# Kernel tuning notes

Hardware: AMD Instinct MI355X
Metric: run time of the kernel (lower is better)

The kernel has to match this reference:

```python
import jax, jax.numpy as jnp
import numpy as np

B, S, D = 8, 1024, 1024
H, KV, HD = 16, 16, 64
NDIM = 2
EPS = 1e-6


def rms_norm(x, weight=None, eps=EPS):
    var = jnp.mean(jnp.square(x), axis=-1, keepdims=True)
    out = x * jax.lax.rsqrt(var + eps)
    if weight is not None:
        out = out * weight
    return out


def rotate_half(x):
    half = x.shape[-1] // 2
    return jnp.concatenate((-x[..., half:], x[..., :half]), axis=-1)


def multidim_rope(x, cos, sin, ndim):
    # x: [B,S,H,HD]; cos,sin: [B,S,HD]; head_dim split into ndim contiguous
    # chunks of size per = 2*(HD // (2*ndim)); rotate-half applied per chunk.
    b, s, h, hd = x.shape
    per = 2 * (hd // (2 * ndim))
    xg = x.reshape(b, s, h, ndim, per)
    cg = cos.reshape(b, s, 1, ndim, per)
    sg = sin.reshape(b, s, 1, ndim, per)
    out = xg * cg + rotate_half(xg) * sg
    return out.reshape(b, s, h, hd)


def setup_inputs() -> dict:
    key = jax.random.key(0)
    ks = jax.random.split(key, 10)
    scale = 1.0 / np.sqrt(D)
    return {
        "hidden_states": jax.random.normal(ks[0], (B, S, D), jnp.float32),
        "cos": jax.random.uniform(ks[1], (B, S, HD), jnp.float32, -1.0, 1.0),
        "sin": jax.random.uniform(ks[2], (B, S, HD), jnp.float32, -1.0, 1.0),
        "position_ids": jax.random.randint(ks[3], (B, S, NDIM), 0, 32, jnp.int32),
        "wq": jax.random.normal(ks[4], (D, H * HD), jnp.float32) * scale,
        "wk": jax.random.normal(ks[5], (D, KV * HD), jnp.float32) * scale,
        "wv": jax.random.normal(ks[6], (D, KV * HD), jnp.float32) * scale,
        "wo": jax.random.normal(ks[7], (H * HD, D), jnp.float32) * scale,
        "q_norm_w": jnp.ones((HD,), jnp.float32),
        "k_norm_w": jnp.ones((HD,), jnp.float32),
    }


def reference(hidden_states, cos, sin, position_ids, wq, wk, wv, wo, q_norm_w, k_norm_w):
    b, s, _ = hidden_states.shape
    ndim = position_ids.shape[-1]

    q = (hidden_states @ wq).reshape(b, s, H, HD)
    q = rms_norm(q, q_norm_w)
    q = multidim_rope(q, cos, sin, ndim)

    k = (hidden_states @ wk).reshape(b, s, KV, HD)
    k = rms_norm(k, k_norm_w)
    k = multidim_rope(k, cos, sin, ndim)

    v = (hidden_states @ wv).reshape(b, s, KV, HD)
    v = rms_norm(v, None)  # v_norm has no weight

    # Full (non-causal) vision attention, scaling = 1.0
    scores = jnp.einsum("bqhd,bkhd->bhqk", q, k)
    probs = jax.nn.softmax(scores, axis=-1)
    attn = jnp.einsum("bhqk,bkhd->bqhd", probs, v).reshape(b, s, H * HD)

    return attn @ wo
```

## Files before the change

### kernel.cpp

```cpp
#include <hip/hip_runtime.h>
#include <hip/hip_bf16.h>

typedef __attribute__((ext_vector_type(8))) short bf16x8;
typedef __attribute__((ext_vector_type(4))) short bf16x4;
typedef __attribute__((ext_vector_type(4))) float f32x4;

struct __align__(16) V16 { unsigned long long a, b; };

__device__ __forceinline__ float bf2f(unsigned short u) {
  union { unsigned int i; float f; } c; c.i = ((unsigned int)u) << 16; return c.f;
}
__device__ __forceinline__ unsigned short f2bf(float f) {
  unsigned int u; __builtin_memcpy(&u, &f, 4);
  u += 0x7FFFu + ((u >> 16) & 1u);
  return (unsigned short)(u >> 16);
}

__device__ __forceinline__ void async16(unsigned short* lds,
                                        const unsigned short* g) {
  __builtin_amdgcn_global_load_lds(
      (const __attribute__((address_space(1))) unsigned int*)g,
      (__attribute__((address_space(3))) unsigned int*)lds, 16, 0, 0);
}

__device__ __forceinline__ void xcd_swizzle(int& bx, int& by) {
  const int nx = (int)gridDim.x;
  const int nwg = nx * (int)gridDim.y;
  if ((nwg & 7) == 0) {
    int orig = by * nx + bx;
    int swz = (orig & 7) * (nwg >> 3) + (orig >> 3);
    bx = swz % nx;
    by = swz / nx;
  }
}

#define FP32_MAGIC 0x3F800000u

__device__ __forceinline__ void cvt_seg(
    const void* __restrict__ src, unsigned short* __restrict__ dst,
    int n4, int i, int stride, bool f32)
{
  if (f32) {
    const float* s = (const float*)src;
    for (; i < n4; i += stride) {
      float4 v = *(const float4*)(s + (size_t)i * 4);
      ushort2 lo = { f2bf(v.x), f2bf(v.y) };
      ushort2 hi = { f2bf(v.z), f2bf(v.w) };
      *(ushort2*)(dst + (size_t)i * 4)     = lo;
      *(ushort2*)(dst + (size_t)i * 4 + 2) = hi;
    }
  } else {
    const unsigned short* s = (const unsigned short*)src;
    for (; i < n4; i += stride)
      *(ushort4*)(dst + (size_t)i * 4) = *(const ushort4*)(s + (size_t)i * 4);
  }
}

__global__ __launch_bounds__(256) void cvt_bf16(
    const void* __restrict__ src, size_t srcOff,
    unsigned short* __restrict__ dst, int n4,
    const unsigned int* __restrict__ fmt)
{
  const bool f32 = (fmt[0] == FP32_MAGIC);
  const int i = blockIdx.x * blockDim.x + threadIdx.x;
  const int stride = gridDim.x * blockDim.x;
  const void* s = f32 ? (const void*)((const float*)src + srcOff)
                      : (const void*)((const unsigned short*)src + srcOff);
  cvt_seg(s, dst, n4, i, stride, f32);
}

__global__ __launch_bounds__(256) void cvt_all(
    const void* __restrict__ hid, const void* __restrict__ cosr,
    const void* __restrict__ sinr, const void* __restrict__ qnw,
    const void* __restrict__ knw,
    unsigned short* __restrict__ hb, unsigned short* __restrict__ csb,
    unsigned short* __restrict__ snb, unsigned short* __restrict__ qnb,
    unsigned short* __restrict__ knb,
    int hidden_n4, const unsigned int* __restrict__ fmt)
{
  const bool f32 = (fmt[0] == FP32_MAGIC);
  const int bx = blockIdx.x, tid = threadIdx.x;
  if (bx < 2048) {
    if (hidden_n4 > 0)
      cvt_seg(hid, hb, hidden_n4, bx * 256 + tid, 2048 * 256, f32);
  } else if (bx < 2176) {
    cvt_seg(cosr, csb, 131072, (bx - 2048) * 256 + tid, 128 * 256, f32);
  } else if (bx < 2304) {
    cvt_seg(sinr, snb, 131072, (bx - 2176) * 256 + tid, 128 * 256, f32);
  } else {
    if (tid < 16)       cvt_seg(qnw, qnb, 16, tid, 16, f32);
    else if (tid < 32)  cvt_seg(knw, knb, 16, tid - 16, 16, f32);
  }
}

__global__ __launch_bounds__(256) void cvt_t4(
    const void* __restrict__ s0, const void* __restrict__ s1,
    const void* __restrict__ s2, const void* __restrict__ s3,
    unsigned short* __restrict__ d0, unsigned short* __restrict__ d1,
    unsigned short* __restrict__ d2, unsigned short* __restrict__ d3,
    const unsigned int* __restrict__ fmt)
{
  __shared__ __align__(16) unsigned short T[64][72];
  const int z = blockIdx.z;
  const void* src = (z == 0) ? s0 : (z == 1) ? s1 : (z == 2) ? s2 : s3;
  unsigned short* dstT = (z == 0) ? d0 : (z == 1) ? d1 : (z == 2) ? d2 : d3;

  const bool f32 = (fmt[0] == FP32_MAGIC);
  const int tid = threadIdx.x;
  const int k0 = blockIdx.x * 64, n0 = blockIdx.y * 64;
  const int rl = tid >> 3, cl = (tid & 7) * 8;

#pragma unroll
  for (int p = 0; p < 2; ++p) {
    int r = rl + p * 32;
    int cs = cl ^ (r & 56);
    if (f32) {
      const float* s = (const float*)src + (size_t)(k0 + r) * 1024 + n0 + cl;
      float4 v0 = *(const float4*)s, v1 = *(const float4*)(s + 4);
      unsigned short* t = &T[r][cs];
      t[0]=f2bf(v0.x); t[1]=f2bf(v0.y); t[2]=f2bf(v0.z); t[3]=f2bf(v0.w);
      t[4]=f2bf(v1.x); t[5]=f2bf(v1.y); t[6]=f2bf(v1.z); t[7]=f2bf(v1.w);
    } else {
      *(V16*)&T[r][cs] = *(const V16*)((const unsigned short*)src +
                                        (size_t)(k0 + r) * 1024 + n0 + cl);
    }
  }
  __syncthreads();

#pragma unroll
  for (int p = 0; p < 2; ++p) {
    int u = tid + p * 256;
    int d = u >> 3, sc = (u & 7) * 8;
    unsigned short tmp[8];
#pragma unroll
    for (int i = 0; i < 8; ++i) tmp[i] = T[sc + i][d ^ sc];
    *(V16*)&dstT[(size_t)(n0 + d) * 1024 + k0 + sc] = *(V16*)tmp;
  }
}

#define TM 128
#define TN 128
#define TK 64
#define GK 1024

__global__ __launch_bounds__(256) void gemm_qkv(
    const unsigned short* __restrict__ A,
    const unsigned short* __restrict__ Bt,
    unsigned short* __restrict__ Cq,
    unsigned short* __restrict__ Ck,
    unsigned short* __restrict__ Cv,
    const unsigned short* __restrict__ cs,
    const unsigned short* __restrict__ sn,
    const unsigned short* __restrict__ qw,
    const unsigned short* __restrict__ kw,
    int M)
{
  __shared__ __align__(16) unsigned short LDSu[2 * TM * TK];
  unsigned short (*As)[TK] = (unsigned short (*)[TK])LDSu;
  unsigned short (*Bs)[TK] = (unsigned short (*)[TK])&LDSu[TM * TK];

  const int tid  = threadIdx.x;
  const int wave = tid >> 6;
  const int lane = tid & 63;
  const int quad = lane >> 4;
  const int l16  = lane & 15;
  const int bm = blockIdx.x * TM;
  const int bn = blockIdx.y * TN;
  const int wm = (wave & 1) * 64;
  const int wn = (wave >> 1) * 64;

  const f32x4 z = {0.f, 0.f, 0.f, 0.f};
  f32x4 acc[4][4];
#pragma unroll
  for (int i = 0; i < 4; ++i)
#pragma unroll
    for (int j = 0; j < 4; ++j) acc[i][j] = z;

  const int lrow = lane >> 3;
  const int gcol = ((lane & 7) ^ lrow) * 8;
  const unsigned short* aP = A  + (size_t)(bm + wave * 8 + lrow) * GK + gcol;
  const unsigned short* bP = Bt + (size_t)(bn + wave * 8 + lrow) * GK + gcol;
  const int cswz = l16 & 7;

  for (int k0 = 0; k0 < GK; k0 += TK) {
#pragma unroll
    for (int p = 0; p < 4; ++p) {
      async16(&As[p * 32 + wave * 8][0], aP + (size_t)p * 32 * GK);
      async16(&Bs[p * 32 + wave * 8][0], bP + (size_t)p * 32 * GK);
    }
    aP += TK; bP += TK;
    __syncthreads();

#pragma unroll
    for (int s = 0; s < 2; ++s) {
      const int pc = ((s * 4 + quad) ^ cswz) * 8;
      bf16x8 af[4], bfv[4];
#pragma unroll
      for (int mt = 0; mt < 4; ++mt)
        af[mt] = *(const bf16x8*)&As[wm + mt * 16 + l16][pc];
#pragma unroll
      for (int nt = 0; nt < 4; ++nt)
        bfv[nt] = *(const bf16x8*)&Bs[wn + nt * 16 + l16][pc];
#pragma unroll
      for (int mt = 0; mt < 4; ++mt)
#pragma unroll
        for (int nt = 0; nt < 4; ++nt)
          acc[mt][nt] = __builtin_amdgcn_mfma_f32_16x16x32_bf16(
              af[mt], bfv[nt], acc[mt][nt], 0, 0, 0);
    }
    __syncthreads();
  }

  const int which = bn >> 10;
  const int colbase = (bn & 1023) + wn;

  if (which == 2) {
    unsigned short* Tw = LDSu + wave * 4096;
#pragma unroll
    for (int mt = 0; mt < 4; ++mt)
#pragma unroll
      for (int r = 0; r < 4; ++r) {
        const int s = mt * 16 + quad * 4 + r;
        float x0 = acc[mt][0][r], x1 = acc[mt][1][r];
        float x2 = acc[mt][2][r], x3 = acc[mt][3][r];
        float ss = x0 * x0 + x1 * x1 + x2 * x2 + x3 * x3;
        ss += __shfl_xor(ss, 1);
        ss += __shfl_xor(ss, 2);
        ss += __shfl_xor(ss, 4);
        ss += __shfl_xor(ss, 8);
        const float inv = rsqrtf(ss * (1.f / 64.f) + 1e-6f);
        const int sw = (s >> 3) << 3;
#pragma unroll
        for (int nt = 0; nt < 4; ++nt)
          Tw[s * 64 + ((nt * 16 + l16) ^ sw)] = f2bf(acc[mt][nt][r] * inv);
      }
    __builtin_amdgcn_wave_barrier();

    const int vhead = ((bm >> 10) * 16 + (colbase >> 6)) * 64;
    const int sbase = (bm & 1023) + wm;
    const int sg = (lane & 7) * 8;
    const int dl = lane >> 3;
#pragma unroll
    for (int p = 0; p < 8; ++p) {
      const int d = p * 8 + dl;
      unsigned short tmp[8];
#pragma unroll
      for (int i = 0; i < 8; ++i)
        tmp[i] = Tw[(sg + i) * 64 + (d ^ sg)];
      *(V16*)&Cv[(size_t)(vhead + d) * 1024 + sbase + sg] = *(V16*)tmp;
    }
    return;
  }

  unsigned short* Cd = (which == 0) ? Cq : Ck;
  float wgt[4];
#pragma unroll
  for (int nt = 0; nt < 4; ++nt) {
    int d = nt * 16 + l16;
    wgt[nt] = (which == 0) ? bf2f(qw[d]) * 1.44269504f : bf2f(kw[d]);
  }

#pragma unroll
  for (int mt = 0; mt < 4; ++mt)
#pragma unroll
    for (int r = 0; r < 4; ++r) {
      const int row = bm + wm + mt * 16 + quad * 4 + r;
      float x0 = acc[mt][0][r], x1 = acc[mt][1][r];
      float x2 = acc[mt][2][r], x3 = acc[mt][3][r];
      float ss = x0 * x0 + x1 * x1 + x2 * x2 + x3 * x3;
      ss += __shfl_xor(ss, 1);
      ss += __shfl_xor(ss, 2);
      ss += __shfl_xor(ss, 4);
      ss += __shfl_xor(ss, 8);
      const float inv = rsqrtf(ss * (1.f / 64.f) + 1e-6f);
      float y[4] = { x0 * inv * wgt[0], x1 * inv * wgt[1],
                     x2 * inv * wgt[2], x3 * inv * wgt[3] };
      const unsigned short* cp = cs + (size_t)row * 64 + l16;
      const unsigned short* sp = sn + (size_t)row * 64 + l16;
#pragma unroll
      for (int nt = 0; nt < 4; ++nt) {
        float c = bf2f(cp[nt * 16]), s = bf2f(sp[nt * 16]);
        float part = (nt & 1) ? y[nt ^ 1] : -y[nt ^ 1];
        Cd[(size_t)row * 1024 + colbase + nt * 16 + l16] =
            f2bf(y[nt] * c + part * s);
      }
    }
}

__global__ __launch_bounds__(256) void gemm_bf16(
    const unsigned short* __restrict__ A,
    const unsigned short* __restrict__ Bt,
    void* __restrict__ C, size_t cOff,
    const unsigned int* __restrict__ outFmt,
    int M, int N)
{
  __shared__ __align__(16) unsigned short As[TM][TK];
  __shared__ __align__(16) unsigned short Bs[TN][TK];

  const int tid  = threadIdx.x;
  const int wave = tid >> 6;
  const int lane = tid & 63;
  const int quad = lane >> 4;
  const int l16  = lane & 15;
  const int bm = blockIdx.x * TM;
  const int bn = blockIdx.y * TN;
  const int wm = (wave & 1) * 64;
  const int wn = (wave >> 1) * 64;

  const f32x4 z = {0.f, 0.f, 0.f, 0.f};
  f32x4 acc[4][4];
#pragma unroll
  for (int i = 0; i < 4; ++i)
#pragma unroll
    for (int j = 0; j < 4; ++j) acc[i][j] = z;

  const int lrow = lane >> 3;
  const int gcol = ((lane & 7) ^ lrow) * 8;
  const unsigned short* aP = A  + (size_t)(bm + wave * 8 + lrow) * GK + gcol;
  const unsigned short* bP = Bt + (size_t)(bn + wave * 8 + lrow) * GK + gcol;
  const int cswz = l16 & 7;

  for (int k0 = 0; k0 < GK; k0 += TK) {
#pragma unroll
    for (int p = 0; p < 4; ++p) {
      async16(&As[p * 32 + wave * 8][0], aP + (size_t)p * 32 * GK);
      async16(&Bs[p * 32 + wave * 8][0], bP + (size_t)p * 32 * GK);
    }
    aP += TK; bP += TK;
    __syncthreads();

#pragma unroll
    for (int s = 0; s < 2; ++s) {
      const int pc = ((s * 4 + quad) ^ cswz) * 8;
      bf16x8 af[4], bfv[4];
#pragma unroll
      for (int mt = 0; mt < 4; ++mt)
        af[mt] = *(const bf16x8*)&As[wm + mt * 16 + l16][pc];
#pragma unroll
      for (int nt = 0; nt < 4; ++nt)
        bfv[nt] = *(const bf16x8*)&Bs[wn + nt * 16 + l16][pc];
#pragma unroll
      for (int mt = 0; mt < 4; ++mt)
#pragma unroll
        for (int nt = 0; nt < 4; ++nt)
          acc[mt][nt] = __builtin_amdgcn_mfma_f32_16x16x32_bf16(
              af[mt], bfv[nt], acc[mt][nt], 0, 0, 0);
    }
    __syncthreads();
  }

  const bool of32 = (outFmt != nullptr) && (outFmt[0] == FP32_MAGIC);
  float* Cf = (float*)C + cOff;
  unsigned short* Ch = (unsigned short*)C + cOff;

#pragma unroll
  for (int mt = 0; mt < 4; ++mt)
#pragma unroll
    for (int nt = 0; nt < 4; ++nt)
#pragma unroll
      for (int r = 0; r < 4; ++r) {
        int row = bm + wm + mt * 16 + quad * 4 + r;
        int col = bn + wn + nt * 16 + l16;
        size_t idx = (size_t)row * N + col;
        if (of32) Cf[idx] = acc[mt][nt][r];
        else      Ch[idx] = f2bf(acc[mt][nt][r]);
      }
}

__global__ __launch_bounds__(256, 3) void attn_fused(
    const unsigned short* __restrict__ q,
    const unsigned short* __restrict__ k,
    const unsigned short* __restrict__ vt,
    unsigned short* __restrict__ o)
{
  __shared__ __align__(16) unsigned short Ks[2][64][64];
  __shared__ __align__(16) unsigned short Vs[2][64][64];

  int bxs = blockIdx.x, bys = blockIdx.y;
  xcd_swizzle(bxs, bys);

  const int tid  = threadIdx.x;
  const int wave = tid >> 6;
  const int lane = tid & 63;
  const int quad = lane >> 4;
  const int l16  = lane & 15;
  const int bh = bys;
  const int b  = bh >> 4, h = bh & 15;
  const int qbase = bxs * 128 + wave * 32;
  const size_t bbase = (size_t)b * 1024;

  bf16x8 qfA[2], qfB[2];
  {
    const unsigned short* qp = q + (bbase + qbase + l16) * 1024 + h * 64;
    qfA[0] = *(const bf16x8*)(qp + quad * 8);
    qfA[1] = *(const bf16x8*)(qp + 32 + quad * 8);
    qfB[0] = *(const bf16x8*)(qp + 16 * 1024 + quad * 8);
    qfB[1] = *(const bf16x8*)(qp + 16 * 1024 + 32 + quad * 8);
  }

  const f32x4 z = {0.f, 0.f, 0.f, 0.f};
  f32x4 ofA[5], ofB[5];
#pragma unroll
  for (int nt = 0; nt < 5; ++nt) { ofA[nt] = z; ofB[nt] = z; }
  float mA = -1e30f, mB = -1e30f;

  const bf16x8 onesv = { 0x3F80, 0x3F80, 0x3F80, 0x3F80,
                         0x3F80, 0x3F80, 0x3F80, 0x3F80 };

  const int lrow = lane >> 3;
  const int gcol = ((lane & 7) ^ lrow) * 8;
  const unsigned short* kP = k  + (bbase + wave * 8 + lrow) * 1024 + h * 64 + gcol;
  const unsigned short* vP = vt + ((size_t)bh * 64 + wave * 8 + lrow) * 1024 + gcol;
  const int cswz = l16 & 7;

  auto STAGE = [&](int buf, int kt) {
#pragma unroll
    for (int p = 0; p < 2; ++p) {
      async16(&Ks[buf][p * 32 + wave * 8][0], kP + ((size_t)kt * 64 + p * 32) * 1024);
      async16(&Vs[buf][p * 32 + wave * 8][0], vP + (size_t)p * 32 * 1024 + kt * 64);
    }
  };

  STAGE(0, 0);
  __syncthreads();

#pragma unroll 2
  for (int kt = 0; kt < 16; ++kt) {
    const int cur = kt & 1;
    if (kt < 15) STAGE(cur ^ 1, kt + 1);

    f32x4 sA[4], sB[4];
#pragma unroll
    for (int nt = 0; nt < 4; ++nt) { sA[nt] = z; sB[nt] = z; }
    __builtin_amdgcn_s_setprio(1);
#pragma unroll
    for (int s = 0; s < 2; ++s) {
      const int pc = ((s * 4 + quad) ^ cswz) * 8;
#pragma unroll
      for (int nt = 0; nt < 4; ++nt) {
        bf16x8 kf = *(const bf16x8*)&Ks[cur][nt * 16 + l16][pc];
        sA[nt] = __builtin_amdgcn_mfma_f32_16x16x32_bf16(kf, qfA[s], sA[nt], 0, 0, 0);
        sB[nt] = __builtin_amdgcn_mfma_f32_16x16x32_bf16(kf, qfB[s], sB[nt], 0, 0, 0);
      }
    }
    __builtin_amdgcn_s_setprio(0);

    float mxA, mxB;
    {
      float a0 = fmaxf(fmaxf(sA[0][0], sA[0][1]), fmaxf(sA[0][2], sA[0][3]));
      float a1 = fmaxf(fmaxf(sA[1][0], sA[1][1]), fmaxf(sA[1][2], sA[1][3]));
      float a2 = fmaxf(fmaxf(sA[2][0], sA[2][1]), fmaxf(sA[2][2], sA[2][3]));
      float a3 = fmaxf(fmaxf(sA[3][0], sA[3][1]), fmaxf(sA[3][2], sA[3][3]));
      mxA = fmaxf(fmaxf(a0, a1), fmaxf(a2, a3));
      mxA = fmaxf(mxA, __shfl_xor(mxA, 16));
      mxA = fmaxf(mxA, __shfl_xor(mxA, 32));
      float b0 = fmaxf(fmaxf(sB[0][0], sB[0][1]), fmaxf(sB[0][2], sB[0][3]));
      float b1 = fmaxf(fmaxf(sB[1][0], sB[1][1]), fmaxf(sB[1][2], sB[1][3]));
      float b2 = fmaxf(fmaxf(sB[2][0], sB[2][1]), fmaxf(sB[2][2], sB[2][3]));
      float b3 = fmaxf(fmaxf(sB[3][0], sB[3][1]), fmaxf(sB[3][2], sB[3][3]));
      mxB = fmaxf(fmaxf(b0, b1), fmaxf(b2, b3));
      mxB = fmaxf(mxB, __shfl_xor(mxB, 16));
      mxB = fmaxf(mxB, __shfl_xor(mxB, 32));
    }

    if (!__all((mxA - mA <= 11.5f) && (mxB - mB <= 11.5f))) {
      float mnA = fmaxf(mA, mxA);
      float mnB = fmaxf(mB, mxB);
      float aA = __builtin_amdgcn_exp2f(mA - mnA);
      float aB = __builtin_amdgcn_exp2f(mB - mnB);
      mA = mnA; mB = mnB;
      float arA[4], arB[4];
#pragma unroll
      for (int r = 0; r < 4; ++r) {
        arA[r] = __shfl(aA, quad * 4 + r);
        arB[r] = __shfl(aB, quad * 4 + r);
      }
#pragma unroll
      for (int nt = 0; nt < 5; ++nt)
#pragma unroll
        for (int r = 0; r < 4; ++r) {
          ofA[nt][r] *= arA[r];
          ofB[nt][r] *= arB[r];
        }
    }

    bf16x8 pA[2], pB[2];
#pragma unroll
    for (int nt = 0; nt < 4; ++nt)
#pragma unroll
      for (int r = 0; r < 4; ++r) {
        pA[nt >> 1][(nt & 1) * 4 + r] =
            (short)f2bf(__builtin_amdgcn_exp2f(sA[nt][r] - mA));
        pB[nt >> 1][(nt & 1) * 4 + r] =
            (short)f2bf(__builtin_amdgcn_exp2f(sB[nt][r] - mB));
      }

    __builtin_amdgcn_s_setprio(1);
#pragma unroll
    for (int s = 0; s < 2; ++s) {
#pragma unroll
      for (int nt = 0; nt < 4; ++nt) {
        const unsigned short* vrow = &Vs[cur][nt * 16 + l16][0];
        const int g0  = (4 * s + (quad >> 1)) ^ cswz;
        const int off = 4 * (quad & 1);
        bf16x4 v0 = *(const bf16x4*)(vrow + g0 * 8 + off);
        bf16x4 v1 = *(const bf16x4*)(vrow + (g0 ^ 2) * 8 + off);
        bf16x8 vf = __builtin_shufflevector(v0, v1, 0, 1, 2, 3, 4, 5, 6, 7);
        ofA[nt] = __builtin_amdgcn_mfma_f32_16x16x32_bf16(pA[s], vf, ofA[nt], 0, 0, 0);
        ofB[nt] = __builtin_amdgcn_mfma_f32_16x16x32_bf16(pB[s], vf, ofB[nt], 0, 0, 0);
      }
      ofA[4] = __builtin_amdgcn_mfma_f32_16x16x32_bf16(pA[s], onesv, ofA[4], 0, 0, 0);
      ofB[4] = __builtin_amdgcn_mfma_f32_16x16x32_bf16(pB[s], onesv, ofB[4], 0, 0, 0);
    }
    __builtin_amdgcn_s_setprio(0);

    __syncthreads();
  }

  float ilA[4], ilB[4];
#pragma unroll
  for (int r = 0; r < 4; ++r) {
    ilA[r] = 1.f / ofA[4][r];
    ilB[r] = 1.f / ofB[4][r];
  }
#pragma unroll
  for (int nt = 0; nt < 4; ++nt)
#pragma unroll
    for (int r = 0; r < 4; ++r) {
      int row = qbase + quad * 4 + r;
      o[(bbase + row) * 1024 + h * 64 + nt * 16 + l16] = f2bf(ofA[nt][r] * ilA[r]);
      o[(bbase + row + 16) * 1024 + h * 64 + nt * 16 + l16] = f2bf(ofB[nt][r] * ilB[r]);
    }
}

extern "C" void kernel_launch(void* const* d_in, const int* in_sizes, int n_in,
                              void* d_out, int out_size, void* d_ws, size_t ws_size,
                              hipStream_t stream) {
  const void* hidden = d_in[0];
  const void* cosr   = d_in[1];
  const void* sinr   = d_in[2];
  const void* wq     = d_in[4];
  const void* wk     = d_in[5];
  const void* wv     = d_in[6];
  const void* wo     = d_in[7];
  const void* qnw    = d_in[8];
  const void* knw    = d_in[9];
  const unsigned int* fmt = (const unsigned int*)qnw;

  const size_t MEG = 1024 * 1024;
  dim3 blk(256);
  unsigned short* w = (unsigned short*)d_ws;

  if (ws_size >= (size_t)60 * MEG) {
    unsigned short* hb   = w;
    unsigned short* wqT  = w + 8 * MEG;
    unsigned short* wkT  = w + 9 * MEG;
    unsigned short* wvT  = w + 10 * MEG;
    unsigned short* woT  = w + 11 * MEG;
    unsigned short* csb  = w + 12 * MEG;
    unsigned short* snb  = w + 12 * MEG + 512 * 1024;
    unsigned short* qnb  = w + 13 * MEG;
    unsigned short* knb  = w + 13 * MEG + 64;
    unsigned short* qb   = w + 14 * MEG;
    unsigned short* kb   = w + 22 * MEG;
    unsigned short* vtb  = (unsigned short*)d_out;
    unsigned short* ab   = qb;

    cvt_all<<<dim3(2305), blk, 0, stream>>>(hidden, cosr, sinr, qnw, knw,
                                            hb, csb, snb, qnb, knb,
                                            2 * (int)MEG, fmt);
    cvt_t4<<<dim3(16, 16, 4), blk, 0, stream>>>(wq, wk, wv, wo,
                                                wqT, wkT, wvT, woT, fmt);

    const int M = 8192;
    gemm_qkv<<<dim3(M / TM, 24), blk, 0, stream>>>(hb, wqT, qb, kb, vtb,
                                                   csb, snb, qnb, knb, M);
    attn_fused<<<dim3(8, 8 * 16), blk, 0, stream>>>(qb, kb, vtb, ab);
    gemm_bf16<<<dim3(M / TM, 8), blk, 0, stream>>>(ab, woT, d_out, 0, fmt,
                                                   M, 1024);
  } else {
    unsigned short* wqT  = w;
    unsigned short* wkT  = w + 1 * MEG;
    unsigned short* wvT  = w + 2 * MEG;
    unsigned short* woT  = w + 3 * MEG;
    unsigned short* csb  = w + 4 * MEG;
    unsigned short* snb  = w + 4 * MEG + 512 * 1024;
    unsigned short* qnb  = w + 5 * MEG;
    unsigned short* knb  = w + 5 * MEG + 64;
    unsigned short* hbb  = w + 6 * MEG;
    unsigned short* qb   = w + 7 * MEG;
    unsigned short* kb   = w + 8 * MEG;
    unsigned short* vtb  = w + 10 * MEG;

    cvt_t4<<<dim3(16, 16, 4), blk, 0, stream>>>(wq, wk, wv, wo,
                                                wqT, wkT, wvT, woT, fmt);
    cvt_all<<<dim3(2305), blk, 0, stream>>>(hidden, cosr, sinr, qnw, knw,
                                            nullptr, csb, snb, qnb, knb,
                                            0, fmt);

    const int Mb = 1024;
    for (int b = 0; b < 8; ++b) {
      cvt_bf16<<<dim3(512), blk, 0, stream>>>(hidden, (size_t)b * MEG, hbb,
                                              (int)(MEG / 4), fmt);
      gemm_qkv<<<dim3(Mb / TM, 24), blk, 0, stream>>>(
          hbb, wqT, qb, kb, vtb, csb + (size_t)b * 64 * 1024,
          snb + (size_t)b * 64 * 1024, qnb, knb, Mb);
      attn_fused<<<dim3(8, 16), blk, 0, stream>>>(qb, kb, vtb, qb);
      gemm_bf16<<<dim3(Mb / TM, 8), blk, 0, stream>>>(qb, woT, d_out,
                                                      (size_t)b * MEG, fmt,
                                                      Mb, 1024);
    }
  }
}
```

Measured before the change: 256.0 us.

## Restructure QKV GEMM into 256x128 tiles with double-buffered async LDS pipeline

The fused QKV projection kernel moves from 128x128 tiles with 4 waves to 256x128 tiles with 8 waves. It adds a double-buffered LDS pipeline that issues the next K-slice's async global-to-LDS loads in two halves, interleaved with the MFMA phases, using explicit vmcnt waits and barriers. MFMA sections are wrapped in s_setprio. The aim is to hide global load latency behind compute and raise B-tile reuse, at the cost of more LDS (96KB) and hand-managed wait counts that must match the number of in-flight loads.

```diff
diff --git a/kernel.cpp b/kernel.cpp
--- a/kernel.cpp
+++ b/kernel.cpp
@@ -138,12 +138,12 @@
   }
 }
 
-#define TM 128
-#define TN 128
 #define TK 64
 #define GK 1024
-
-__global__ __launch_bounds__(256) void gemm_qkv(
+#define QTM 256
+#define QTN 128
+
+__global__ __launch_bounds__(512, 2) void gemm_qkv(
     const unsigned short* __restrict__ A,
     const unsigned short* __restrict__ Bt,
     unsigned short* __restrict__ Cq,
@@ -155,19 +155,17 @@
     const unsigned short* __restrict__ kw,
     int M)
 {
-  __shared__ __align__(16) unsigned short LDSu[2 * TM * TK];
-  unsigned short (*As)[TK] = (unsigned short (*)[TK])LDSu;
-  unsigned short (*Bs)[TK] = (unsigned short (*)[TK])&LDSu[TM * TK];
+  __shared__ __align__(16) unsigned short LDSu[2 * (QTM + QTN) * TK];
 
   const int tid  = threadIdx.x;
   const int wave = tid >> 6;
   const int lane = tid & 63;
   const int quad = lane >> 4;
   const int l16  = lane & 15;
-  const int bm = blockIdx.x * TM;
-  const int bn = blockIdx.y * TN;
-  const int wm = (wave & 1) * 64;
-  const int wn = (wave >> 1) * 64;
+  const int wr   = wave >> 1;
+  const int wc   = wave & 1;
+  const int bm = blockIdx.x * QTM;
+  const int bn = blockIdx.y * QTN;
 
   const f32x4 z = {0.f, 0.f, 0.f, 0.f};
   f32x4 acc[4][4];
@@ -182,37 +180,74 @@
   const unsigned short* bP = Bt + (size_t)(bn + wave * 8 + lrow) * GK + gcol;
   const int cswz = l16 & 7;
 
-  for (int k0 = 0; k0 < GK; k0 += TK) {
-#pragma unroll
-    for (int p = 0; p < 4; ++p) {
-      async16(&As[p * 32 + wave * 8][0], aP + (size_t)p * 32 * GK);
-      async16(&Bs[p * 32 + wave * 8][0], bP + (size_t)p * 32 * GK);
-    }
-    aP += TK; bP += TK;
-    __syncthreads();
-
-#pragma unroll
-    for (int s = 0; s < 2; ++s) {
-      const int pc = ((s * 4 + quad) ^ cswz) * 8;
-      bf16x8 af[4], bfv[4];
+  unsigned short* As0 = LDSu;
+  unsigned short* Bs0 = LDSu + QTM * TK;
+  const int BUFS = (QTM + QTN) * TK;
+
+  auto STAGE_A = [&](int b, int t, int p) {
+    async16(As0 + b * BUFS + (p * 64 + wave * 8) * TK,
+            aP + (size_t)(p * 64) * GK + t * TK);
+  };
+  auto STAGE_B = [&](int b, int t, int p) {
+    async16(Bs0 + b * BUFS + (p * 64 + wave * 8) * TK,
+            bP + (size_t)(p * 64) * GK + t * TK);
+  };
+
+  STAGE_A(0, 0, 0); STAGE_A(0, 0, 1); STAGE_A(0, 0, 2); STAGE_A(0, 0, 3);
+  STAGE_B(0, 0, 0); STAGE_B(0, 0, 1);
+
+#pragma unroll 2
+  for (int t = 0; t < 16; ++t) {
+    const int cur = t & 1, nxt = cur ^ 1;
+
+    if (t < 15) {
+      STAGE_A(nxt, t + 1, 0); STAGE_A(nxt, t + 1, 1); STAGE_B(nxt, t + 1, 0);
+      asm volatile("s_waitcnt vmcnt(3)" ::: "memory");
+    } else {
+      asm volatile("s_waitcnt vmcnt(0)" ::: "memory");
+    }
+    asm volatile("s_barrier" ::: "memory");
+
+    const unsigned short* Ab = As0 + cur * BUFS;
+    const unsigned short* Bb = Bs0 + cur * BUFS;
+    bf16x8 af[4][2], bfv[4][2];
+#pragma unroll
+    for (int ks = 0; ks < 2; ++ks) {
+      const int pc = ((ks * 4 + quad) ^ cswz) * 8;
 #pragma unroll
       for (int mt = 0; mt < 4; ++mt)
-        af[mt] = *(const bf16x8*)&As[wm + mt * 16 + l16][pc];
+        af[mt][ks] = *(const bf16x8*)&Ab[(wr * 64 + mt * 16 + l16) * TK + pc];
 #pragma unroll
       for (int nt = 0; nt < 4; ++nt)
-        bfv[nt] = *(const bf16x8*)&Bs[wn + nt * 16 + l16][pc];
-#pragma unroll
-      for (int mt = 0; mt < 4; ++mt)
-#pragma unroll
-        for (int nt = 0; nt < 4; ++nt)
-          acc[mt][nt] = __builtin_amdgcn_mfma_f32_16x16x32_bf16(
-              af[mt], bfv[nt], acc[mt][nt], 0, 0, 0);
-    }
-    __syncthreads();
+        bfv[nt][ks] = *(const bf16x8*)&Bb[(wc * 64 + nt * 16 + l16) * TK + pc];
+    }
+
+    __builtin_amdgcn_s_setprio(1);
+#pragma unroll
+    for (int mt = 0; mt < 4; ++mt)
+#pragma unroll
+      for (int nt = 0; nt < 4; ++nt)
+        acc[mt][nt] = __builtin_amdgcn_mfma_f32_16x16x32_bf16(
+            af[mt][0], bfv[nt][0], acc[mt][nt], 0, 0, 0);
+    __builtin_amdgcn_s_setprio(0);
+    asm volatile("s_barrier" ::: "memory");
+
+    if (t < 15) {
+      STAGE_A(nxt, t + 1, 2); STAGE_A(nxt, t + 1, 3); STAGE_B(nxt, t + 1, 1);
+    }
+    __builtin_amdgcn_s_setprio(1);
+#pragma unroll
+    for (int mt = 0; mt < 4; ++mt)
+#pragma unroll
+      for (int nt = 0; nt < 4; ++nt)
+        acc[mt][nt] = __builtin_amdgcn_mfma_f32_16x16x32_bf16(
+            af[mt][1], bfv[nt][1], acc[mt][nt], 0, 0, 0);
+    __builtin_amdgcn_s_setprio(0);
+    asm volatile("s_barrier" ::: "memory");
   }
 
   const int which = bn >> 10;
-  const int colbase = (bn & 1023) + wn;
+  const int colbase = (bn & 1023) + wc * 64;
 
   if (which == 2) {
     unsigned short* Tw = LDSu + wave * 4096;
@@ -237,7 +272,7 @@
     __builtin_amdgcn_wave_barrier();
 
     const int vhead = ((bm >> 10) * 16 + (colbase >> 6)) * 64;
-    const int sbase = (bm & 1023) + wm;
+    const int sbase = (bm & 1023) + wr * 64;
     const int sg = (lane & 7) * 8;
     const int dl = lane >> 3;
 #pragma unroll
@@ -264,7 +299,7 @@
   for (int mt = 0; mt < 4; ++mt)
 #pragma unroll
     for (int r = 0; r < 4; ++r) {
-      const int row = bm + wm + mt * 16 + quad * 4 + r;
+      const int row = bm + wr * 64 + mt * 16 + quad * 4 + r;
       float x0 = acc[mt][0][r], x1 = acc[mt][1][r];
       float x2 = acc[mt][2][r], x3 = acc[mt][3][r];
       float ss = x0 * x0 + x1 * x1 + x2 * x2 + x3 * x3;
@@ -286,6 +321,9 @@
       }
     }
 }
+
+#define TM 128
+#define TN 128
 
 __global__ __launch_bounds__(256) void gemm_bf16(
     const unsigned short* __restrict__ A,
@@ -549,6 +587,7 @@
 
   const size_t MEG = 1024 * 1024;
   dim3 blk(256);
+  dim3 blk512(512);
   unsigned short* w = (unsigned short*)d_ws;
 
   if (ws_size >= (size_t)60 * MEG) {
@@ -573,8 +612,8 @@
                                                 wqT, wkT, wvT, woT, fmt);
 
     const int M = 8192;
-    gemm_qkv<<<dim3(M / TM, 24), blk, 0, stream>>>(hb, wqT, qb, kb, vtb,
-                                                   csb, snb, qnb, knb, M);
+    gemm_qkv<<<dim3(M / QTM, 24), blk512, 0, stream>>>(hb, wqT, qb, kb, vtb,
+                                                       csb, snb, qnb, knb, M);
     attn_fused<<<dim3(8, 8 * 16), blk, 0, stream>>>(qb, kb, vtb, ab);
     gemm_bf16<<<dim3(M / TM, 8), blk, 0, stream>>>(ab, woT, d_out, 0, fmt,
                                                    M, 1024);
@@ -602,7 +641,7 @@
     for (int b = 0; b < 8; ++b) {
       cvt_bf16<<<dim3(512), blk, 0, stream>>>(hidden, (size_t)b * MEG, hbb,
                                               (int)(MEG / 4), fmt);
-      gemm_qkv<<<dim3(Mb / TM, 24), blk, 0, stream>>>(
+      gemm_qkv<<<dim3(Mb / QTM, 24), blk512, 0, stream>>>(
           hbb, wqT, qb, kb, vtb, csb + (size_t)b * 64 * 1024,
           snb + (size_t)b * 64 * 1024, qnb, knb, Mb);
       attn_fused<<<dim3(8, 16), blk, 0, stream>>>(qb, kb, vtb, qb);
```

Result: no change. 251.7 us (-1.7%).
